# Kernel tuning notes

Hardware: AMD Instinct MI355X
Metric: run time of the kernel (lower is better)

The kernel has to match this reference:

```python
import jax, jax.numpy as jnp
import numpy as np

VOCAB, EMB_DIM = 50000, 300
HIDDEN, OUT_DIM, N_ASPECTS = 256, 3, 8
BATCH, SEQ = 8192, 128


def setup_inputs() -> dict:
    key = jax.random.key(0)
    k1, k2, k3, k4, k5, k6, k7 = jax.random.split(key, 7)
    input_ids = jax.random.randint(k1, (BATCH, SEQ), 0, VOCAB, dtype=jnp.int64 if jax.config.jax_enable_x64 else jnp.int32)
    aspect_id = jax.random.randint(k2, (BATCH,), 0, N_ASPECTS, dtype=jnp.int32)
    emb = jax.random.normal(k3, (VOCAB, EMB_DIM), dtype=jnp.float32)
    # Per-aspect 2-layer MLP params, stacked along aspect axis. PyTorch Linear
    # init scale ~ U(-1/sqrt(fan_in), 1/sqrt(fan_in)).
    s1 = 1.0 / np.sqrt(EMB_DIM)
    s2 = 1.0 / np.sqrt(HIDDEN)
    W1 = jax.random.uniform(k4, (N_ASPECTS, EMB_DIM, HIDDEN), jnp.float32, -s1, s1)
    b1 = jax.random.uniform(k5, (N_ASPECTS, HIDDEN), jnp.float32, -s1, s1)
    W2 = jax.random.uniform(k6, (N_ASPECTS, HIDDEN, OUT_DIM), jnp.float32, -s2, s2)
    b2 = jax.random.uniform(k7, (N_ASPECTS, OUT_DIM), jnp.float32, -s2, s2)
    return {"input_ids": input_ids, "aspect_id": aspect_id, "emb": emb,
            "W1": W1, "b1": b1, "W2": W2, "b2": b2}


def reference(input_ids, aspect_id, emb, W1, b1, W2, b2):
    # Embedding lookup + mean-pool over sequence -> [B, EMB_DIM]
    x = emb[input_ids].mean(axis=1)
    # Run every sample through every aspect MLP (A is tiny: 8), then select.
    # Same math as per-sample routed MLP, but as A batched GEMMs.
    h = jax.nn.relu(jnp.einsum('bd,adh->abh', x, W1) + b1[:, None, :])  # [A,B,H]
    o = jnp.einsum('abh,aho->abo', h, W2) + b2[:, None, :]              # [A,B,O]
    # Select per-sample expert output: [B, OUT_DIM]
    o_b = jnp.transpose(o, (1, 0, 2))  # [B, A, O]
    return jnp.take_along_axis(o_b, aspect_id[:, None, None], axis=1)[:, 0, :]
```

## Files before the change

kernel.cpp:

```cpp
#include <hip/hip_runtime.h>

constexpr int EMB_DIM   = 300;
constexpr int HIDDEN    = 256;
constexpr int OUT_DIM   = 3;
constexpr int SEQ       = 128;
constexpr int N_ASPECTS = 8;
constexpr int TILE      = 32;
constexpr int MTILE     = 16;

__device__ __forceinline__ unsigned int bfbits(float f) {
  unsigned int u = __float_as_uint(f);
  return (u + 0x7fffu + ((u >> 16) & 1u)) >> 16;
}
__device__ __forceinline__ unsigned int pack2(float lo, float hi) {
  return bfbits(lo) | (bfbits(hi) << 16);
}
__device__ __forceinline__ float blo(unsigned int u) { return __uint_as_float(u << 16); }
__device__ __forceinline__ float bhi(unsigned int u) { return __uint_as_float(u & 0xffff0000u); }

__global__ __launch_bounds__(1024) void prep_kernel(
    const float* __restrict__ emb, unsigned int* __restrict__ emb16, int n8,
    const int* __restrict__ aspect, int B, int* __restrict__ perm, int nperm) {
  const int t = threadIdx.x;

  if (blockIdx.x != 0) {
    int i = (blockIdx.x - 1) * 1024 + t;
    const int stride = (gridDim.x - 1) * 1024;
    for (; i < n8; i += stride) {
      const float4* p = (const float4*)emb + (size_t)i * 2;
      float4 a = p[0], b = p[1];
      uint4 o;
      o.x = pack2(a.x, a.y); o.y = pack2(a.z, a.w);
      o.z = pack2(b.x, b.y); o.w = pack2(b.z, b.w);
      ((uint4*)emb16)[i] = o;
    }
    return;
  }

  const int lane = t & 63, wave = t >> 6;
  __shared__ int wcnt[16][N_ASPECTS];
  __shared__ int cur[16][N_ASPECTS];

  for (int i = t; i < nperm; i += 1024) perm[i] = -1;

  int my_a[8];
  int cnt[N_ASPECTS];
#pragma unroll
  for (int q = 0; q < N_ASPECTS; ++q) cnt[q] = 0;
#pragma unroll
  for (int k = 0; k < 8; ++k) {
    int s = t + k * 1024;
    int a = (s < B) ? aspect[s] : -1;
    my_a[k] = a;
#pragma unroll
    for (int q = 0; q < N_ASPECTS; ++q) cnt[q] += (a == q);
  }
#pragma unroll
  for (int q = 0; q < N_ASPECTS; ++q) {
    int c = cnt[q];
    for (int off = 32; off > 0; off >>= 1) c += __shfl_down(c, off);
    if (lane == 0) wcnt[wave][q] = c;
  }
  __syncthreads();
  if (t == 0) {
    int base = 0;
    for (int q = 0; q < N_ASPECTS; ++q) {
      int tot = 0;
      for (int w = 0; w < 16; ++w) { cur[w][q] = base + tot; tot += wcnt[w][q]; }
      base += ((tot + TILE - 1) / TILE) * TILE;
    }
  }
  __syncthreads();

#pragma unroll
  for (int k = 0; k < 8; ++k) {
    int a = my_a[k];
    int s = t + k * 1024;
#pragma unroll
    for (int q = 0; q < N_ASPECTS; ++q) {
      unsigned long long m = __ballot(a == q);
      if (a == q) {
        int rank = __popcll(m & ((1ull << lane) - 1ull));
        int pos = cur[wave][q] + rank;
        perm[pos] = s;
        if (rank == __popcll(m) - 1) cur[wave][q] = pos + 1;
      }
    }
  }
}

__global__ __launch_bounds__(256) void pool_kernel(
    const int* __restrict__ ids, const unsigned short* __restrict__ emb16,
    float* __restrict__ x, int B) {
  const int wave = threadIdx.x >> 6, lane = threadIdx.x & 63;
  const int b = blockIdx.x * 4 + wave;
  if (b >= B) return;

  int r0 = ids[(size_t)b * SEQ + lane];
  int r1 = ids[(size_t)b * SEQ + lane + 64];

#pragma unroll
  for (int k = 2; k <= 128; k <<= 1) {
#pragma unroll
    for (int j = k >> 1; j >= 1; j >>= 1) {
      if (j == 64) {
        int lo = min(r0, r1), hi = max(r0, r1);
        r0 = lo; r1 = hi;
      } else {
        const bool up0 = ((lane & k) == 0);
        const bool up1 = (((lane + 64) & k) == 0);
        const bool side = ((lane & j) == 0);
        int o0 = __shfl_xor(r0, j);
        int o1 = __shfl_xor(r1, j);
        r0 = (side == up0) ? min(r0, o0) : max(r0, o0);
        r1 = (side == up1) ? min(r1, o1) : max(r1, o1);
      }
    }
  }

  __shared__ int sid[4][SEQ];
  sid[wave][lane]      = r0;
  sid[wave][lane + 64] = r1;
  __syncthreads();

  float a0 = 0.f, a1 = 0.f, a2 = 0.f, a3 = 0.f;
  float c0 = 0.f, c1 = 0.f, c2 = 0.f, c3 = 0.f;
#pragma unroll 4
  for (int s = 0; s < SEQ; ++s) {
    const uint2* __restrict__ r =
        (const uint2*)(emb16 + (size_t)sid[wave][s] * EMB_DIM);
    uint2 v = r[lane];
    a0 += blo(v.x); a1 += bhi(v.x); a2 += blo(v.y); a3 += bhi(v.y);
    if (lane < 11) {
      uint2 w = r[64 + lane];
      c0 += blo(w.x); c1 += bhi(w.x); c2 += blo(w.y); c3 += bhi(w.y);
    }
  }
  const float sc = 1.0f / (float)SEQ;
  float4* __restrict__ xr = (float4*)(x + (size_t)b * EMB_DIM);
  xr[lane] = make_float4(a0 * sc, a1 * sc, a2 * sc, a3 * sc);
  if (lane < 11)
    xr[64 + lane] = make_float4(c0 * sc, c1 * sc, c2 * sc, c3 * sc);
}

__global__ __launch_bounds__(256) void mlp_kernel(
    const float* __restrict__ x, const int* __restrict__ aspect,
    const int* __restrict__ perm,
    const float* __restrict__ W1, const float* __restrict__ b1,
    const float* __restrict__ W2, const float* __restrict__ b2,
    float* __restrict__ out) {
  const int t = threadIdx.x;
  const int wave = t >> 6, lane = t & 63;
  const int g = wave >> 1;
  const int kw = wave & 1;
  const int start = blockIdx.x * MTILE;

  __shared__ int ss[MTILE];
  __shared__ float xch[2][8][64][4];

  if (t < MTILE) ss[t] = perm[start + t];
  __syncthreads();
  const int s0 = ss[0];
  if (s0 < 0) return;
  const int a = aspect[s0];

  int smp[8];
  const float* xrow[8];
#pragma unroll
  for (int s = 0; s < 8; ++s) {
    int m = __builtin_amdgcn_readfirstlane(ss[g * 8 + s]);
    smp[s] = m;
    xrow[s] = x + (size_t)(m < 0 ? s0 : m) * EMB_DIM;
  }

  const float4* __restrict__ w1r =
      (const float4*)(W1 + (size_t)a * EMB_DIM * HIDDEN) + lane;
  float4 acc[8];
  if (kw == 0) {
    const float4 bb = ((const float4*)(b1 + a * HIDDEN))[lane];
#pragma unroll
    for (int s = 0; s < 8; ++s) acc[s] = bb;
  } else {
#pragma unroll
    for (int s = 0; s < 8; ++s) acc[s] = make_float4(0.f, 0.f, 0.f, 0.f);
  }
  const int d0 = kw ? 160 : 0;
  const int d1 = kw ? EMB_DIM : 160;
  for (int d = d0; d < d1; d += 4) {
    float4 xv[8];
#pragma unroll
    for (int s = 0; s < 8; ++s) xv[s] = *(const float4*)(xrow[s] + d);
#pragma unroll
    for (int dd = 0; dd < 4; ++dd) {
      const float4 w = w1r[(size_t)(d + dd) * (HIDDEN / 4)];
#pragma unroll
      for (int s = 0; s < 8; ++s) {
        const float xs = dd == 0 ? xv[s].x : dd == 1 ? xv[s].y
                        : dd == 2 ? xv[s].z : xv[s].w;
        acc[s].x = fmaf(xs, w.x, acc[s].x);
        acc[s].y = fmaf(xs, w.y, acc[s].y);
        acc[s].z = fmaf(xs, w.z, acc[s].z);
        acc[s].w = fmaf(xs, w.w, acc[s].w);
      }
    }
  }

  if (kw == 0) {
#pragma unroll
    for (int i = 0; i < 4; ++i)
      *(float4*)&xch[g][4 + i][lane][0] = acc[4 + i];
  } else {
#pragma unroll
    for (int i = 0; i < 4; ++i)
      *(float4*)&xch[g][i][lane][0] = acc[i];
  }
  __syncthreads();

  const float4* __restrict__ w2p =
      (const float4*)(W2 + (size_t)a * HIDDEN * OUT_DIM + lane * 12);
  const float4 w2a = w2p[0];
  const float4 w2b = w2p[1];
  const float4 w2c = w2p[2];

  float4 own[4];
  int ms[4];
  if (kw == 0) {
    own[0] = acc[0]; own[1] = acc[1]; own[2] = acc[2]; own[3] = acc[3];
    ms[0] = smp[0]; ms[1] = smp[1]; ms[2] = smp[2]; ms[3] = smp[3];
  } else {
    own[0] = acc[4]; own[1] = acc[5]; own[2] = acc[6]; own[3] = acc[7];
    ms[0] = smp[4]; ms[1] = smp[5]; ms[2] = smp[6]; ms[3] = smp[7];
  }
  const int mys = 4 * kw;

  float p[4][OUT_DIM];
#pragma unroll
  for (int i = 0; i < 4; ++i) {
    const float4 pr = *(const float4*)&xch[g][mys + i][lane][0];
    const float h0 = fmaxf(own[i].x + pr.x, 0.f);
    const float h1 = fmaxf(own[i].y + pr.y, 0.f);
    const float h2 = fmaxf(own[i].z + pr.z, 0.f);
    const float h3 = fmaxf(own[i].w + pr.w, 0.f);
    p[i][0] = fmaf(h0, w2a.x, fmaf(h1, w2a.w, fmaf(h2, w2b.z, h3 * w2c.y)));
    p[i][1] = fmaf(h0, w2a.y, fmaf(h1, w2b.x, fmaf(h2, w2b.w, h3 * w2c.z)));
    p[i][2] = fmaf(h0, w2a.z, fmaf(h1, w2b.y, fmaf(h2, w2c.x, h3 * w2c.w)));
  }
#pragma unroll
  for (int off = 32; off > 0; off >>= 1)
#pragma unroll
    for (int i = 0; i < 4; ++i) {
      p[i][0] += __shfl_down(p[i][0], off);
      p[i][1] += __shfl_down(p[i][1], off);
      p[i][2] += __shfl_down(p[i][2], off);
    }

  if (lane == 0) {
    const float g0 = b2[a * OUT_DIM + 0];
    const float g1 = b2[a * OUT_DIM + 1];
    const float g2 = b2[a * OUT_DIM + 2];
#pragma unroll
    for (int i = 0; i < 4; ++i) {
      if (ms[i] >= 0) {
        float* o = out + (size_t)ms[i] * OUT_DIM;
        o[0] = p[i][0] + g0;
        o[1] = p[i][1] + g1;
        o[2] = p[i][2] + g2;
      }
    }
  }
}

extern "C" void kernel_launch(void* const* d_in, const int* in_sizes, int n_in,
                              void* d_out, int out_size, void* d_ws, size_t ws_size,
                              hipStream_t stream) {
  const int*   ids    = (const int*)d_in[0];
  const int*   aspect = (const int*)d_in[1];
  const float* emb    = (const float*)d_in[2];
  const float* W1     = (const float*)d_in[3];
  const float* b1     = (const float*)d_in[4];
  const float* W2     = (const float*)d_in[5];
  const float* b2     = (const float*)d_in[6];
  float*       out    = (float*)d_out;

  const int B     = in_sizes[1];
  const int nemb  = in_sizes[2];
  const int nblk  = (B + TILE - 1) / TILE + N_ASPECTS;
  const int nperm = nblk * TILE;

  float* x    = (float*)d_ws;
  int*   perm = (int*)((char*)d_ws + (size_t)B * EMB_DIM * sizeof(float));
  unsigned short* emb16 =
      (unsigned short*)((char*)perm + (((size_t)nperm * 4 + 15) & ~(size_t)15));

  prep_kernel<<<513, 1024, 0, stream>>>(emb, (unsigned int*)emb16, nemb / 8,
                                        aspect, B, perm, nperm);
  pool_kernel<<<(B + 3) / 4, 256, 0, stream>>>(ids, emb16, x, B);
  mlp_kernel<<<nperm / MTILE, 256, 0, stream>>>(x, aspect, perm, W1, b1, W2, b2, out);
}
```

Before: 131.4 us.

## Split bf16 embedding table into aligned 256-wide and 64-wide padded arrays

The prep kernel now writes the bf16 embedding copy as two separate tables: the first 256 columns at a 512-byte row stride and the remaining 44 columns padded to a 128-byte stride. Rows therefore start on aligned boundaries and addresses come from precomputed shifts. The pool kernel gathers the main part with one full-wave pass. The tail is handled by 44 lanes that each cover a different token, then combined with shuffle reductions, instead of 11 lanes sitting in the main loop. This targets misaligned and poorly coalesced gathers and idle lanes, at the cost of extra workspace and a conversion loop that processes one row per wave.

```diff
diff --git a/kernel.cpp b/kernel.cpp
--- a/kernel.cpp
+++ b/kernel.cpp
@@ -19,25 +19,31 @@
 __device__ __forceinline__ float bhi(unsigned int u) { return __uint_as_float(u & 0xffff0000u); }
 
 __global__ __launch_bounds__(1024) void prep_kernel(
-    const float* __restrict__ emb, unsigned int* __restrict__ emb16, int n8,
+    const float* __restrict__ emb, unsigned short* __restrict__ embA,
+    unsigned short* __restrict__ embB, int vocab,
     const int* __restrict__ aspect, int B, int* __restrict__ perm, int nperm) {
   const int t = threadIdx.x;
+  const int lane = t & 63, wave = t >> 6;
 
   if (blockIdx.x != 0) {
-    int i = (blockIdx.x - 1) * 1024 + t;
-    const int stride = (gridDim.x - 1) * 1024;
-    for (; i < n8; i += stride) {
-      const float4* p = (const float4*)emb + (size_t)i * 2;
-      float4 a = p[0], b = p[1];
-      uint4 o;
-      o.x = pack2(a.x, a.y); o.y = pack2(a.z, a.w);
-      o.z = pack2(b.x, b.y); o.w = pack2(b.z, b.w);
-      ((uint4*)emb16)[i] = o;
+    const int cw = (blockIdx.x - 1) * 16 + wave;
+    const int nw = (gridDim.x - 1) * 16;
+    for (int v = cw; v < vocab; v += nw) {
+      const float4* __restrict__ src = (const float4*)(emb + (size_t)v * EMB_DIM);
+      float4 p = src[lane];
+      uint2 w;
+      w.x = pack2(p.x, p.y); w.y = pack2(p.z, p.w);
+      ((uint2*)(embA + (size_t)v * 256))[lane] = w;
+      if (lane < 11) {
+        float4 q = src[64 + lane];
+        uint2 u;
+        u.x = pack2(q.x, q.y); u.y = pack2(q.z, q.w);
+        ((uint2*)(embB + (size_t)v * 64))[lane] = u;
+      }
     }
     return;
   }
 
-  const int lane = t & 63, wave = t >> 6;
   __shared__ int wcnt[16][N_ASPECTS];
   __shared__ int cur[16][N_ASPECTS];
 
@@ -90,8 +96,8 @@
 }
 
 __global__ __launch_bounds__(256) void pool_kernel(
-    const int* __restrict__ ids, const unsigned short* __restrict__ emb16,
-    float* __restrict__ x, int B) {
+    const int* __restrict__ ids, const unsigned short* __restrict__ embA,
+    const unsigned short* __restrict__ embB, float* __restrict__ x, int B) {
   const int wave = threadIdx.x >> 6, lane = threadIdx.x & 63;
   const int b = blockIdx.x * 4 + wave;
   if (b >= B) return;
@@ -118,29 +124,45 @@
     }
   }
 
-  __shared__ int sid[4][SEQ];
-  sid[wave][lane]      = r0;
-  sid[wave][lane + 64] = r1;
+  __shared__ int sA[4][SEQ];
+  __shared__ int sB[4][SEQ];
+  sA[wave][lane]      = r0 << 9;
+  sA[wave][lane + 64] = r1 << 9;
+  sB[wave][lane]      = r0 << 7;
+  sB[wave][lane + 64] = r1 << 7;
   __syncthreads();
 
   float a0 = 0.f, a1 = 0.f, a2 = 0.f, a3 = 0.f;
+  const char* __restrict__ baseA = (const char*)embA + (size_t)lane * 8;
+#pragma unroll 8
+  for (int s = 0; s < SEQ; ++s) {
+    uint2 v = *(const uint2*)(baseA + sA[wave][s]);
+    a0 += blo(v.x); a1 += bhi(v.x); a2 += blo(v.y); a3 += bhi(v.y);
+  }
+
+  const int myTok = lane / 11;
+  const int mySub = lane - myTok * 11;
   float c0 = 0.f, c1 = 0.f, c2 = 0.f, c3 = 0.f;
-#pragma unroll 4
-  for (int s = 0; s < SEQ; ++s) {
-    const uint2* __restrict__ r =
-        (const uint2*)(emb16 + (size_t)sid[wave][s] * EMB_DIM);
-    uint2 v = r[lane];
-    a0 += blo(v.x); a1 += bhi(v.x); a2 += blo(v.y); a3 += bhi(v.y);
-    if (lane < 11) {
-      uint2 w = r[64 + lane];
-      c0 += blo(w.x); c1 += bhi(w.x); c2 += blo(w.y); c3 += bhi(w.y);
-    }
-  }
+  if (lane < 44) {
+    const char* __restrict__ baseB = (const char*)embB + (size_t)mySub * 8;
+#pragma unroll 8
+    for (int s = 0; s < SEQ; s += 4) {
+      uint2 v = *(const uint2*)(baseB + sB[wave][s + myTok]);
+      c0 += blo(v.x); c1 += bhi(v.x); c2 += blo(v.y); c3 += bhi(v.y);
+    }
+  }
+  c0 += __shfl_down(c0, 22); c1 += __shfl_down(c1, 22);
+  c2 += __shfl_down(c2, 22); c3 += __shfl_down(c3, 22);
+  c0 += __shfl_down(c0, 11); c1 += __shfl_down(c1, 11);
+  c2 += __shfl_down(c2, 11); c3 += __shfl_down(c3, 11);
+
   const float sc = 1.0f / (float)SEQ;
   float4* __restrict__ xr = (float4*)(x + (size_t)b * EMB_DIM);
   xr[lane] = make_float4(a0 * sc, a1 * sc, a2 * sc, a3 * sc);
-  if (lane < 11)
-    xr[64 + lane] = make_float4(c0 * sc, c1 * sc, c2 * sc, c3 * sc);
+  if (lane < 11) {
+    float4* __restrict__ xb = (float4*)(x + (size_t)b * EMB_DIM + 256);
+    xb[lane] = make_float4(c0 * sc, c1 * sc, c2 * sc, c3 * sc);
+  }
 }
 
 __global__ __launch_bounds__(256) void mlp_kernel(
@@ -284,16 +306,18 @@
 
   const int B     = in_sizes[1];
   const int nemb  = in_sizes[2];
+  const int VOCAB = nemb / EMB_DIM;
   const int nblk  = (B + TILE - 1) / TILE + N_ASPECTS;
   const int nperm = nblk * TILE;
 
   float* x    = (float*)d_ws;
   int*   perm = (int*)((char*)d_ws + (size_t)B * EMB_DIM * sizeof(float));
-  unsigned short* emb16 =
-      (unsigned short*)((char*)perm + (((size_t)nperm * 4 + 15) & ~(size_t)15));
-
-  prep_kernel<<<513, 1024, 0, stream>>>(emb, (unsigned int*)emb16, nemb / 8,
+  size_t offA = ((size_t)B * EMB_DIM * sizeof(float) + (size_t)nperm * 4 + 511) & ~(size_t)511;
+  unsigned short* embA = (unsigned short*)((char*)d_ws + offA);
+  unsigned short* embB = embA + (size_t)VOCAB * 256;
+
+  prep_kernel<<<513, 1024, 0, stream>>>(emb, embA, embB, VOCAB,
                                         aspect, B, perm, nperm);
-  pool_kernel<<<(B + 3) / 4, 256, 0, stream>>>(ids, emb16, x, B);
+  pool_kernel<<<(B + 3) / 4, 256, 0, stream>>>(ids, embA, embB, x, B);
   mlp_kernel<<<nperm / MTILE, 256, 0, stream>>>(x, aspect, perm, W1, b1, W2, b2, out);
 }
```

Measured after the change: 135.9 us. 3.4% more time.

## Split pooling into two vocab-range passes for embedding cache locality

Applied to the files above, without the earlier changes.

Runs the pooling kernel twice. Each pass only gathers embedding rows whose sorted token id falls in one half of the vocabulary, and the second pass accumulates into x. The aim is to shrink each pass's working set of the bf16 embedding table (about 15 MB per half) so it fits better in L2 or the last-level cache and raises the gather hit rate. In exchange, the id sort is done twice, there is an extra read-modify-write of x, and there is one more kernel launch.

```diff
diff --git a/kernel.cpp b/kernel.cpp
--- a/kernel.cpp
+++ b/kernel.cpp
@@ -91,7 +91,7 @@
 
 __global__ __launch_bounds__(256) void pool_kernel(
     const int* __restrict__ ids, const unsigned short* __restrict__ emb16,
-    float* __restrict__ x, int B) {
+    float* __restrict__ x, int B, int lo, int hi, int first) {
   const int wave = threadIdx.x >> 6, lane = threadIdx.x & 63;
   const int b = blockIdx.x * 4 + wave;
   if (b >= B) return;
@@ -104,8 +104,8 @@
 #pragma unroll
     for (int j = k >> 1; j >= 1; j >>= 1) {
       if (j == 64) {
-        int lo = min(r0, r1), hi = max(r0, r1);
-        r0 = lo; r1 = hi;
+        int t0 = min(r0, r1), t1 = max(r0, r1);
+        r0 = t0; r1 = t1;
       } else {
         const bool up0 = ((lane & k) == 0);
         const bool up1 = (((lane + 64) & k) == 0);
@@ -118,6 +118,9 @@
     }
   }
 
+  const int s0 = __popcll(__ballot(r0 < lo)) + __popcll(__ballot(r1 < lo));
+  const int s1 = __popcll(__ballot(r0 < hi)) + __popcll(__ballot(r1 < hi));
+
   __shared__ int sid[4][SEQ];
   sid[wave][lane]      = r0;
   sid[wave][lane + 64] = r1;
@@ -126,7 +129,7 @@
   float a0 = 0.f, a1 = 0.f, a2 = 0.f, a3 = 0.f;
   float c0 = 0.f, c1 = 0.f, c2 = 0.f, c3 = 0.f;
 #pragma unroll 4
-  for (int s = 0; s < SEQ; ++s) {
+  for (int s = s0; s < s1; ++s) {
     const uint2* __restrict__ r =
         (const uint2*)(emb16 + (size_t)sid[wave][s] * EMB_DIM);
     uint2 v = r[lane];
@@ -138,9 +141,23 @@
   }
   const float sc = 1.0f / (float)SEQ;
   float4* __restrict__ xr = (float4*)(x + (size_t)b * EMB_DIM);
-  xr[lane] = make_float4(a0 * sc, a1 * sc, a2 * sc, a3 * sc);
-  if (lane < 11)
-    xr[64 + lane] = make_float4(c0 * sc, c1 * sc, c2 * sc, c3 * sc);
+  if (first) {
+    xr[lane] = make_float4(a0 * sc, a1 * sc, a2 * sc, a3 * sc);
+    if (lane < 11) {
+      float4* __restrict__ xb = (float4*)(x + (size_t)b * EMB_DIM + 256);
+      xb[lane - 64 + 64] = make_float4(c0 * sc, c1 * sc, c2 * sc, c3 * sc);
+    }
+  } else {
+    float4 prev = xr[lane];
+    xr[lane] = make_float4(prev.x + a0 * sc, prev.y + a1 * sc,
+                           prev.z + a2 * sc, prev.w + a3 * sc);
+    if (lane < 11) {
+      float4* __restrict__ xb = (float4*)(x + (size_t)b * EMB_DIM + 256);
+      float4 pb = xb[lane];
+      xb[lane] = make_float4(pb.x + c0 * sc, pb.y + c1 * sc,
+                             pb.z + c2 * sc, pb.w + c3 * sc);
+    }
+  }
 }
 
 __global__ __launch_bounds__(256) void mlp_kernel(
@@ -284,6 +301,7 @@
 
   const int B     = in_sizes[1];
   const int nemb  = in_sizes[2];
+  const int VOCAB = nemb / EMB_DIM;
   const int nblk  = (B + TILE - 1) / TILE + N_ASPECTS;
   const int nperm = nblk * TILE;
 
@@ -294,6 +312,10 @@
 
   prep_kernel<<<513, 1024, 0, stream>>>(emb, (unsigned int*)emb16, nemb / 8,
                                         aspect, B, perm, nperm);
-  pool_kernel<<<(B + 3) / 4, 256, 0, stream>>>(ids, emb16, x, B);
+  const int vmid = VOCAB / 2;
+  pool_kernel<<<(B + 3) / 4, 256, 0, stream>>>(ids, emb16, x, B,
+                                               0, vmid, 1);
+  pool_kernel<<<(B + 3) / 4, 256, 0, stream>>>(ids, emb16, x, B,
+                                               vmid, 0x7fffffff, 0);
   mlp_kernel<<<nperm / MTILE, 256, 0, stream>>>(x, aspect, perm, W1, b1, W2, b2, out);
 }
```

Measured after the change: 146.5 us. +11.5%, slower.
